# Kernel tuning notes

Measured on AMD Instinct MI355X. Metric: run time of the kernel, lower is better.

The kernel has to match this reference:

```python
import jax, jax.numpy as jnp
import numpy as np

N = 100000
NFEAT = 512
NHID = 256
NCLASS = 40
E = 1600000
K = 10          # nlayers propagation hops
ALPHA = 0.1


def setup_inputs() -> dict:
    key = jax.random.key(0)
    ks = jax.random.split(key, 8)
    x = jax.random.normal(ks[0], (N, NFEAT), dtype=jnp.float32)
    edge_src = jax.random.randint(ks[1], (E,), 0, N, dtype=jnp.int32)
    edge_dst = jax.random.randint(ks[2], (E,), 0, N, dtype=jnp.int32)
    # roughly row-stochastic-scale edge values (avg degree ~16)
    edge_val = jax.random.uniform(ks[3], (E,), dtype=jnp.float32) * (1.0 / 16.0)
    stdv1 = 1.0 / np.sqrt(NFEAT)
    W1 = jax.random.uniform(ks[4], (NFEAT, NHID), minval=-stdv1, maxval=stdv1, dtype=jnp.float32)
    b1 = jax.random.uniform(ks[5], (NHID,), minval=-stdv1, maxval=stdv1, dtype=jnp.float32)
    stdv2 = 1.0 / np.sqrt(NHID)
    W2 = jax.random.uniform(ks[6], (NHID, NCLASS), minval=-stdv2, maxval=stdv2, dtype=jnp.float32)
    b2 = jax.random.uniform(ks[7], (NCLASS,), minval=-stdv2, maxval=stdv2, dtype=jnp.float32)
    return {"x": x, "edge_src": edge_src, "edge_dst": edge_dst, "edge_val": edge_val,
            "W1": W1, "b1": b1, "W2": W2, "b2": b2}


def _spmm(edge_src, edge_dst, edge_val, z):
    # sparse adj @ z via gather + segment-sum scatter: out[dst] += val * z[src]
    msgs = edge_val[:, None] * z[edge_src]          # [E, C]
    return jax.ops.segment_sum(msgs, edge_dst, num_segments=N)


def reference(x, edge_src, edge_dst, edge_val, W1, b1, W2, b2):
    # MLP transform (dropout is identity in eval mode)
    h = jax.nn.relu(x @ W1 + b1)                    # [N, NHID]
    h = h @ W2 + b2                                 # [N, NCLASS]
    # APPNP propagation: z <- (1-alpha) * A z + alpha * h
    def step(z, _):
        z = _spmm(edge_src, edge_dst, edge_val, z) * (1.0 - ALPHA) + ALPHA * h
        return z, None
    z, _ = jax.lax.scan(step, h, None, length=K)
    return jax.nn.log_softmax(z, axis=1)
```

## Files before the change

kernel.cpp:

```cpp
#include <hip/hip_runtime.h>
#include <hip/hip_bf16.h>
#include <math.h>

#define NN     100000
#define NFEATD 512
#define NHIDD  256
#define NCLS   40
#define NE     1600000
#define KHOP   10

typedef __attribute__((ext_vector_type(8))) short short8;
typedef __attribute__((ext_vector_type(4))) float floatx4;

static __device__ __forceinline__ float bf2f(unsigned int u) {
  unsigned int x = u << 16;
  float f;
  __builtin_memcpy(&f, &x, 4);
  return f;
}
static __device__ __forceinline__ unsigned short f2bf(float f) {
  unsigned int x;
  __builtin_memcpy(&x, &f, 4);
  x = (x + 0x7fffu + ((x >> 16) & 1u)) >> 16;
  return (unsigned short)x;
}
static __device__ __forceinline__ void bf8_to_f(const uint4 u, float* f) {
  unsigned int a0 = u.x, a1 = u.y, a2 = u.z, a3 = u.w;
  unsigned int t;
  t = a0 << 16;          __builtin_memcpy(&f[0], &t, 4);
  t = a0 & 0xffff0000u;  __builtin_memcpy(&f[1], &t, 4);
  t = a1 << 16;          __builtin_memcpy(&f[2], &t, 4);
  t = a1 & 0xffff0000u;  __builtin_memcpy(&f[3], &t, 4);
  t = a2 << 16;          __builtin_memcpy(&f[4], &t, 4);
  t = a2 & 0xffff0000u;  __builtin_memcpy(&f[5], &t, 4);
  t = a3 << 16;          __builtin_memcpy(&f[6], &t, 4);
  t = a3 & 0xffff0000u;  __builtin_memcpy(&f[7], &t, 4);
}

__global__ __launch_bounds__(256) void wt_kernel(const float* __restrict__ W1,
                                                 unsigned short* __restrict__ Wt) {
  int i = blockIdx.x * 256 + threadIdx.x;
  int k = i >> 8;
  int n = i & 255;
  Wt[n * 512 + k] = f2bf(W1[i]);
}

__global__ __launch_bounds__(256) void gemm1_mfma_kernel(
    const float* __restrict__ x, const unsigned short* __restrict__ Wt,
    const float* __restrict__ b1, unsigned short* __restrict__ h1) {
  __shared__ unsigned short As[128 * 40];
  __shared__ unsigned short Bs[128 * 40];
  const int tid = threadIdx.x;
  const int lane = tid & 63;
  const int wave = tid >> 6;
  const int wr = wave >> 1, wc = wave & 1;
  const int m = lane & 15, quad = lane >> 4;
  const int c0 = blockIdx.x * 128;
  const int r0 = blockIdx.y * 128;

  const int arow = tid >> 3;
  const int akq = tid & 7;
  const int brow = tid >> 2;
  const int bkq = tid & 3;

  floatx4 acc[4][4];
#pragma unroll
  for (int i = 0; i < 4; ++i)
#pragma unroll
    for (int j = 0; j < 4; ++j) acc[i][j] = (floatx4){0.f, 0.f, 0.f, 0.f};

  float4 aR[4];
  uint4 bR[2];
#pragma unroll
  for (int rep = 0; rep < 4; ++rep) {
    int grow = r0 + arow + rep * 32;
    aR[rep] = make_float4(0.f, 0.f, 0.f, 0.f);
    if (grow < NN) aR[rep] = *(const float4*)(x + grow * NFEATD + akq * 4);
  }
#pragma unroll
  for (int rep = 0; rep < 2; ++rep)
    bR[rep] = *(const uint4*)(Wt + (c0 + brow + rep * 64) * NFEATD + bkq * 8);

  for (int kt = 0; kt < NFEATD; kt += 32) {
#pragma unroll
    for (int rep = 0; rep < 4; ++rep) {
      ushort4 o;
      o.x = f2bf(aR[rep].x);
      o.y = f2bf(aR[rep].y);
      o.z = f2bf(aR[rep].z);
      o.w = f2bf(aR[rep].w);
      *(ushort4*)&As[(arow + rep * 32) * 40 + akq * 4] = o;
    }
#pragma unroll
    for (int rep = 0; rep < 2; ++rep)
      *(uint4*)&Bs[(brow + rep * 64) * 40 + bkq * 8] = bR[rep];
    __syncthreads();

    int ktn = kt + 32;
    if (ktn < NFEATD) {
#pragma unroll
      for (int rep = 0; rep < 4; ++rep) {
        int grow = r0 + arow + rep * 32;
        float4 v = make_float4(0.f, 0.f, 0.f, 0.f);
        if (grow < NN) v = *(const float4*)(x + grow * NFEATD + ktn + akq * 4);
        aR[rep] = v;
      }
#pragma unroll
      for (int rep = 0; rep < 2; ++rep)
        bR[rep] = *(const uint4*)(Wt + (c0 + brow + rep * 64) * NFEATD + ktn + bkq * 8);
    }

    short8 af[4], bfr[4];
#pragma unroll
    for (int i = 0; i < 4; ++i)
      af[i] = *(const short8*)&As[(wr * 64 + i * 16 + m) * 40 + quad * 8];
#pragma unroll
    for (int j = 0; j < 4; ++j)
      bfr[j] = *(const short8*)&Bs[(wc * 64 + j * 16 + m) * 40 + quad * 8];
#pragma unroll
    for (int i = 0; i < 4; ++i)
#pragma unroll
      for (int j = 0; j < 4; ++j)
        acc[i][j] = __builtin_amdgcn_mfma_f32_16x16x32_bf16(af[i], bfr[j], acc[i][j], 0, 0, 0);
    __syncthreads();
  }

  float bias[4];
#pragma unroll
  for (int j = 0; j < 4; ++j) bias[j] = b1[c0 + wc * 64 + j * 16 + m];
#pragma unroll
  for (int i = 0; i < 4; ++i) {
#pragma unroll
    for (int r = 0; r < 4; ++r) {
      int row = r0 + wr * 64 + i * 16 + quad * 4 + r;
      if (row < NN) {
#pragma unroll
        for (int j = 0; j < 4; ++j) {
          float v = acc[i][j][r] + bias[j];
          h1[row * NHIDD + c0 + wc * 64 + j * 16 + m] = f2bf(fmaxf(v, 0.f));
        }
      }
    }
  }
}

__global__ __launch_bounds__(256) void gemm2_kernel(
    const unsigned short* __restrict__ h1, const float* __restrict__ W2,
    const float* __restrict__ b2, unsigned short* __restrict__ hb) {
  __shared__ float w2s[NHIDD * NCLS];
  __shared__ float b2s[NCLS];
  __shared__ unsigned short h1s[64 * 264];
  const int tid = threadIdx.x;
  const int r0 = blockIdx.x * 64;
  for (int i = tid; i < NHIDD * NCLS; i += 256) w2s[i] = W2[i];
  if (tid < NCLS) b2s[tid] = b2[tid];
#pragma unroll
  for (int q = 0; q < 8; ++q) {
    int l = tid + q * 256;
    int lr = l >> 5;
    int lc = (l & 31) << 3;
    int row = r0 + lr;
    uint4 v = make_uint4(0, 0, 0, 0);
    if (row < NN) v = *(const uint4*)(h1 + row * NHIDD + lc);
    *(uint4*)&h1s[lr * 264 + lc] = v;
  }
  __syncthreads();
  const int lr = tid >> 2;
  const int cq = (tid & 3) * 10;
  float acc[10];
#pragma unroll
  for (int j = 0; j < 10; ++j) acc[j] = 0.f;
#pragma unroll 4
  for (int k = 0; k < NHIDD; k += 2) {
    unsigned int hp = *(const unsigned int*)&h1s[lr * 264 + k];
    float a0 = bf2f(hp & 0xffffu);
    float a1 = bf2f(hp >> 16);
    const float* w0 = &w2s[k * NCLS + cq];
    const float* w1 = &w2s[(k + 1) * NCLS + cq];
#pragma unroll
    for (int j = 0; j < 10; ++j)
      acc[j] = fmaf(a1, w1[j], fmaf(a0, w0[j], acc[j]));
  }
  int row = r0 + lr;
  if (row < NN) {
#pragma unroll
    for (int jj = 0; jj < 5; ++jj) {
      unsigned int u = (unsigned int)f2bf(acc[2 * jj] + b2s[cq + 2 * jj]) |
                       ((unsigned int)f2bf(acc[2 * jj + 1] + b2s[cq + 2 * jj + 1]) << 16);
      *(unsigned int*)&hb[row * NCLS + cq + 2 * jj] = u;
    }
  }
}

__global__ __launch_bounds__(256) void zero_kernel(int* __restrict__ p, int n) {
  int i = blockIdx.x * 256 + threadIdx.x;
  if (i < n) p[i] = 0;
}
__global__ __launch_bounds__(256) void count_kernel(const int* __restrict__ edst,
                                                    int* __restrict__ counts) {
  int e = blockIdx.x * 256 + threadIdx.x;
  if (e < NE) atomicAdd(&counts[edst[e]], 1);
}
__global__ __launch_bounds__(256) void hist_kernel(const int* __restrict__ counts,
                                                   int* __restrict__ binoff) {
  __shared__ int lhist[64];
  int tid = threadIdx.x;
  if (tid < 64) lhist[tid] = 0;
  __syncthreads();
  int r = blockIdx.x * 256 + tid;
  if (r < NN) {
    int d = counts[r];
    if (d > 63) d = 63;
    atomicAdd(&lhist[d], 1);
  }
  __syncthreads();
  if (tid < 64) {
    int c = lhist[tid];
    if (c) atomicAdd(&binoff[tid], c);
  }
}
__global__ __launch_bounds__(64) void binscan_kernel(int* __restrict__ binoff) {
  __shared__ int s[64];
  int t = threadIdx.x;
  s[t] = binoff[t];
  __syncthreads();
  if (t == 0) {
    int run = 0;
    for (int i = 0; i < 64; ++i) {
      int c = s[i];
      s[i] = run;
      run += c;
    }
  }
  __syncthreads();
  binoff[t] = s[t];
}
__global__ __launch_bounds__(256) void scatter_rows_kernel(
    const int* __restrict__ counts, int* __restrict__ binoff,
    int* __restrict__ perm, int* __restrict__ spos) {
  __shared__ int lhist[64];
  __shared__ int lbase[64];
  int tid = threadIdx.x;
  if (tid < 64) lhist[tid] = 0;
  __syncthreads();
  int r = blockIdx.x * 256 + tid;
  int d = 0, lrank = 0;
  bool valid = (r < NN);
  if (valid) {
    d = counts[r];
    if (d > 63) d = 63;
    lrank = atomicAdd(&lhist[d], 1);
  }
  __syncthreads();
  if (tid < 64) {
    int c = lhist[tid];
    lbase[tid] = c ? atomicAdd(&binoff[tid], c) : 0;
  }
  __syncthreads();
  if (valid) {
    int pos = lbase[d] + lrank;
    perm[pos] = r;
    spos[r] = pos;
  }
}
__global__ __launch_bounds__(256) void scan_blocks_kernel(
    const int* __restrict__ counts, const int* __restrict__ perm,
    int* __restrict__ srs, int* __restrict__ bsum) {
  __shared__ int s[256];
  int gid = blockIdx.x * 256 + threadIdx.x;
  int v = (gid < NN) ? counts[perm[gid]] : 0;
  s[threadIdx.x] = v;
  __syncthreads();
  for (int off = 1; off < 256; off <<= 1) {
    int t = (threadIdx.x >= off) ? s[threadIdx.x - off] : 0;
    __syncthreads();
    s[threadIdx.x] += t;
    __syncthreads();
  }
  if (gid < NN) srs[gid + 1] = s[threadIdx.x];
  if (threadIdx.x == 255) bsum[blockIdx.x] = s[255];
}
#define NB 391
__global__ __launch_bounds__(512) void scan_sums_kernel(int* __restrict__ bsum) {
  __shared__ int s[512];
  int tid = threadIdx.x;
  int v = (tid < NB) ? bsum[tid] : 0;
  s[tid] = v;
  __syncthreads();
  for (int off = 1; off < 512; off <<= 1) {
    int t = (tid >= off) ? s[tid - off] : 0;
    __syncthreads();
    s[tid] += t;
    __syncthreads();
  }
  if (tid < NB) bsum[tid] = (tid == 0) ? 0 : s[tid - 1];
}
__global__ __launch_bounds__(256) void add_off_kernel(int* __restrict__ srs,
                                                      const int* __restrict__ bsum) {
  int gid = blockIdx.x * 256 + threadIdx.x;
  if (gid < NN) srs[gid + 1] += bsum[blockIdx.x];
  if (gid == 0) srs[0] = 0;
}
__global__ __launch_bounds__(256) void scatter_kernel(
    const int* __restrict__ esrc, const int* __restrict__ edst,
    const float* __restrict__ eval, const int* __restrict__ srs,
    const int* __restrict__ spos, int* __restrict__ cursor,
    int2* __restrict__ csr_pair) {
  int e = blockIdx.x * 256 + threadIdx.x;
  if (e < NE) {
    int p = spos[edst[e]];
    int idx = srs[p] + atomicAdd(&cursor[p], 1);
    csr_pair[idx] = make_int2(esrc[e], __float_as_int(eval[e]));
  }
}

__global__ __launch_bounds__(256) void prop_kernel(
    const int* __restrict__ srs, const int* __restrict__ perm,
    const int2* __restrict__ csr_pair, const unsigned short* __restrict__ zi,
    const unsigned short* __restrict__ hb, unsigned short* __restrict__ zo) {
  int t = blockIdx.x * 256 + threadIdx.x;
  if (t >= NN * 5) return;
  unsigned int p = (unsigned int)t / 5u;
  int cg8 = (t - (int)p * 5) * 8;
  int e0 = srs[p], e1 = srs[p + 1];
  int r = perm[p];
  float acc[8];
#pragma unroll
  for (int j = 0; j < 8; ++j) acc[j] = 0.f;

  int e = e0;
  for (; e + 8 <= e1; e += 8) {
    int2 pr[8];
#pragma unroll
    for (int q = 0; q < 8; ++q) pr[q] = csr_pair[e + q];
    uint4 g[8];
#pragma unroll
    for (int q = 0; q < 8; ++q)
      g[q] = *(const uint4*)(zi + pr[q].x * NCLS + cg8);
#pragma unroll
    for (int q = 0; q < 8; ++q) {
      float zf[8];
      bf8_to_f(g[q], zf);
      float v = __int_as_float(pr[q].y);
#pragma unroll
      for (int j = 0; j < 8; ++j) acc[j] = fmaf(v, zf[j], acc[j]);
    }
  }
  for (; e < e1; ++e) {
    int2 pr = csr_pair[e];
    uint4 g = *(const uint4*)(zi + pr.x * NCLS + cg8);
    float zf[8];
    bf8_to_f(g, zf);
    float v = __int_as_float(pr.y);
#pragma unroll
    for (int j = 0; j < 8; ++j) acc[j] = fmaf(v, zf[j], acc[j]);
  }

  uint4 hu = *(const uint4*)(hb + r * NCLS + cg8);
  float hf[8];
  bf8_to_f(hu, hf);
  uint4 o;
  unsigned int w[4];
#pragma unroll
  for (int i = 0; i < 4; ++i) {
    unsigned int lo = f2bf(0.9f * acc[2 * i] + 0.1f * hf[2 * i]);
    unsigned int hi = f2bf(0.9f * acc[2 * i + 1] + 0.1f * hf[2 * i + 1]);
    w[i] = lo | (hi << 16);
  }
  o.x = w[0];
  o.y = w[1];
  o.z = w[2];
  o.w = w[3];
  *(uint4*)(zo + r * NCLS + cg8) = o;
}

__global__ __launch_bounds__(256) void lsm_kernel(const unsigned short* __restrict__ zf,
                                                  float* __restrict__ out) {
  int r = blockIdx.x * 256 + threadIdx.x;
  if (r >= NN) return;
  float v[NCLS];
#pragma unroll
  for (int q = 0; q < 5; ++q) {
    uint4 u = *(const uint4*)(zf + r * NCLS + q * 8);
    bf8_to_f(u, v + q * 8);
  }
  float m = v[0];
#pragma unroll
  for (int i = 1; i < NCLS; ++i) m = fmaxf(m, v[i]);
  float ssum = 0.f;
#pragma unroll
  for (int i = 0; i < NCLS; ++i) ssum += expf(v[i] - m);
  float lse = m + logf(ssum);
#pragma unroll
  for (int q = 0; q < 10; ++q) {
    float4 o;
    o.x = v[q * 4 + 0] - lse;
    o.y = v[q * 4 + 1] - lse;
    o.z = v[q * 4 + 2] - lse;
    o.w = v[q * 4 + 3] - lse;
    *(float4*)(out + r * NCLS + q * 4) = o;
  }
}

extern "C" void kernel_launch(void* const* d_in, const int* in_sizes, int n_in,
                              void* d_out, int out_size, void* d_ws, size_t ws_size,
                              hipStream_t stream) {
  const float* x = (const float*)d_in[0];
  const int* esrc = (const int*)d_in[1];
  const int* edst = (const int*)d_in[2];
  const float* eval = (const float*)d_in[3];
  const float* W1 = (const float*)d_in[4];
  const float* b1 = (const float*)d_in[5];
  const float* W2 = (const float*)d_in[6];
  const float* b2 = (const float*)d_in[7];
  float* out = (float*)d_out;
  char* ws = (char*)d_ws;

  unsigned short* hb = (unsigned short*)(ws + 0);
  unsigned short* zB0 = (unsigned short*)(ws + 8000000);
  unsigned short* zB1 = (unsigned short*)(ws + 16000000);
  unsigned short* Wt = (unsigned short*)(ws + 24000000);
  unsigned short* h1 = (unsigned short*)(ws + 24400000);
  int* counts = (int*)(ws + 75600000);
  int* cursor = (int*)(ws + 76000000);
  int* srs = (int*)(ws + 76400000);
  int* bsum = (int*)(ws + 76800064);
  int* binoff = (int*)(ws + 76802112);
  int* perm = (int*)(ws + 76802624);
  int* spos = (int*)(ws + 77202624);
  int2* csr_pair = (int2*)(ws + 77602624);

  zero_kernel<<<(2 * NN + 255) / 256, 256, 0, stream>>>(counts, 2 * NN);
  zero_kernel<<<1, 256, 0, stream>>>(binoff, 64);

  wt_kernel<<<(NFEATD * NHIDD) / 256, 256, 0, stream>>>(W1, Wt);
  gemm1_mfma_kernel<<<dim3(2, (NN + 127) / 128), 256, 0, stream>>>(x, Wt, b1, h1);
  gemm2_kernel<<<(NN + 63) / 64, 256, 0, stream>>>(h1, W2, b2, hb);

  count_kernel<<<(NE + 255) / 256, 256, 0, stream>>>(edst, counts);
  hist_kernel<<<(NN + 255) / 256, 256, 0, stream>>>(counts, binoff);
  binscan_kernel<<<1, 64, 0, stream>>>(binoff);
  scatter_rows_kernel<<<(NN + 255) / 256, 256, 0, stream>>>(counts, binoff, perm, spos);
  scan_blocks_kernel<<<NB, 256, 0, stream>>>(counts, perm, srs, bsum);
  scan_sums_kernel<<<1, 512, 0, stream>>>(bsum);
  add_off_kernel<<<NB, 256, 0, stream>>>(srs, bsum);
  scatter_kernel<<<(NE + 255) / 256, 256, 0, stream>>>(esrc, edst, eval, srs, spos,
                                                       cursor, csr_pair);

  const unsigned short* zin = hb;
  unsigned short* zout = zB0;
  for (int i = 0; i < KHOP; ++i) {
    prop_kernel<<<(NN * 5 + 255) / 256, 256, 0, stream>>>(srs, perm, csr_pair,
                                                          zin, hb, zout);
    if (i == 0) {
      zin = zB0;
      zout = zB1;
    } else {
      unsigned short* t = (unsigned short*)zin;
      zin = zout;
      zout = t;
    }
  }

  lsm_kernel<<<(NN + 255) / 256, 256, 0, stream>>>(zB1, out);
}
```

Measured before the change: 1.038 ms.

## Stream GEMM1 operands directly from global memory into MFMA fragments

Measured after the change: 1.072 ms. +3.3%, slower.

```diff
diff --git a/kernel.cpp b/kernel.cpp
--- a/kernel.cpp
+++ b/kernel.cpp
@@ -45,102 +45,107 @@
   Wt[n * 512 + k] = f2bf(W1[i]);
 }
 
-__global__ __launch_bounds__(256) void gemm1_mfma_kernel(
+__global__ __launch_bounds__(256) void gemm1_stream_kernel(
     const float* __restrict__ x, const unsigned short* __restrict__ Wt,
     const float* __restrict__ b1, unsigned short* __restrict__ h1) {
-  __shared__ unsigned short As[128 * 40];
-  __shared__ unsigned short Bs[128 * 40];
+  __shared__ __align__(16) unsigned short hs[128 * 128];
   const int tid = threadIdx.x;
   const int lane = tid & 63;
-  const int wave = tid >> 6;
-  const int wr = wave >> 1, wc = wave & 1;
-  const int m = lane & 15, quad = lane >> 4;
-  const int c0 = blockIdx.x * 128;
-  const int r0 = blockIdx.y * 128;
-
-  const int arow = tid >> 3;
-  const int akq = tid & 7;
-  const int brow = tid >> 2;
-  const int bkq = tid & 3;
-
-  floatx4 acc[4][4];
-#pragma unroll
-  for (int i = 0; i < 4; ++i)
-#pragma unroll
-    for (int j = 0; j < 4; ++j) acc[i][j] = (floatx4){0.f, 0.f, 0.f, 0.f};
-
-  float4 aR[4];
-  uint4 bR[2];
-#pragma unroll
-  for (int rep = 0; rep < 4; ++rep) {
-    int grow = r0 + arow + rep * 32;
-    aR[rep] = make_float4(0.f, 0.f, 0.f, 0.f);
-    if (grow < NN) aR[rep] = *(const float4*)(x + grow * NFEATD + akq * 4);
-  }
-#pragma unroll
-  for (int rep = 0; rep < 2; ++rep)
-    bR[rep] = *(const uint4*)(Wt + (c0 + brow + rep * 64) * NFEATD + bkq * 8);
-
-  for (int kt = 0; kt < NFEATD; kt += 32) {
-#pragma unroll
-    for (int rep = 0; rep < 4; ++rep) {
-      ushort4 o;
-      o.x = f2bf(aR[rep].x);
-      o.y = f2bf(aR[rep].y);
-      o.z = f2bf(aR[rep].z);
-      o.w = f2bf(aR[rep].w);
-      *(ushort4*)&As[(arow + rep * 32) * 40 + akq * 4] = o;
-    }
-#pragma unroll
-    for (int rep = 0; rep < 2; ++rep)
-      *(uint4*)&Bs[(brow + rep * 64) * 40 + bkq * 8] = bR[rep];
-    __syncthreads();
-
-    int ktn = kt + 32;
-    if (ktn < NFEATD) {
-#pragma unroll
-      for (int rep = 0; rep < 4; ++rep) {
-        int grow = r0 + arow + rep * 32;
-        float4 v = make_float4(0.f, 0.f, 0.f, 0.f);
-        if (grow < NN) v = *(const float4*)(x + grow * NFEATD + ktn + akq * 4);
-        aR[rep] = v;
+  const int w = tid >> 6;
+  const int m = lane & 15;
+  const int q = lane >> 4;
+
+  int b = blockIdx.x;
+  int g = b >> 4, slot = b & 15;
+  int xcol = slot >> 3;
+  int y = g * 8 + (slot & 7);
+  if (y >= 782) return;
+  const int r0 = y * 128 + w * 32;
+  const int c0 = xcol * 128;
+
+  const float* arow[2];
+#pragma unroll
+  for (int i = 0; i < 2; ++i) {
+    int gr = r0 + i * 16 + m;
+    arow[i] = x + (size_t)(gr < NN ? gr : 0) * NFEATD + q * 8;
+  }
+  const unsigned short* brow = Wt + (c0 + m) * NFEATD + q * 8;
+
+  floatx4 acc[2][8];
+#pragma unroll
+  for (int i = 0; i < 2; ++i)
+#pragma unroll
+    for (int j = 0; j < 8; ++j) acc[i][j] = (floatx4){0.f, 0.f, 0.f, 0.f};
+
+  float4 apf[2][2][2];
+#pragma unroll
+  for (int par = 0; par < 2; ++par)
+#pragma unroll
+    for (int i = 0; i < 2; ++i) {
+      apf[par][i][0] = *(const float4*)(arow[i] + par * 32);
+      apf[par][i][1] = *(const float4*)(arow[i] + par * 32 + 4);
+    }
+
+#pragma unroll
+  for (int s = 0; s < 16; ++s) {
+    const int par = s & 1;
+    short8 bfr[8];
+#pragma unroll
+    for (int j = 0; j < 8; ++j)
+      bfr[j] = *(const short8*)(brow + j * 16 * NFEATD + s * 32);
+    short8 af[2];
+#pragma unroll
+    for (int i = 0; i < 2; ++i) {
+      float4 lo = apf[par][i][0], hi = apf[par][i][1];
+      short8 t;
+      t[0] = (short)f2bf(lo.x);
+      t[1] = (short)f2bf(lo.y);
+      t[2] = (short)f2bf(lo.z);
+      t[3] = (short)f2bf(lo.w);
+      t[4] = (short)f2bf(hi.x);
+      t[5] = (short)f2bf(hi.y);
+      t[6] = (short)f2bf(hi.z);
+      t[7] = (short)f2bf(hi.w);
+      af[i] = t;
+    }
+    if (s + 2 < 16) {
+#pragma unroll
+      for (int i = 0; i < 2; ++i) {
+        apf[par][i][0] = *(const float4*)(arow[i] + (s + 2) * 32);
+        apf[par][i][1] = *(const float4*)(arow[i] + (s + 2) * 32 + 4);
       }
-#pragma unroll
-      for (int rep = 0; rep < 2; ++rep)
-        bR[rep] = *(const uint4*)(Wt + (c0 + brow + rep * 64) * NFEATD + ktn + bkq * 8);
-    }
-
-    short8 af[4], bfr[4];
-#pragma unroll
-    for (int i = 0; i < 4; ++i)
-      af[i] = *(const short8*)&As[(wr * 64 + i * 16 + m) * 40 + quad * 8];
-#pragma unroll
-    for (int j = 0; j < 4; ++j)
-      bfr[j] = *(const short8*)&Bs[(wc * 64 + j * 16 + m) * 40 + quad * 8];
-#pragma unroll
-    for (int i = 0; i < 4; ++i)
-#pragma unroll
-      for (int j = 0; j < 4; ++j)
-        acc[i][j] = __builtin_amdgcn_mfma_f32_16x16x32_bf16(af[i], bfr[j], acc[i][j], 0, 0, 0);
-    __syncthreads();
-  }
-
-  float bias[4];
-#pragma unroll
-  for (int j = 0; j < 4; ++j) bias[j] = b1[c0 + wc * 64 + j * 16 + m];
-#pragma unroll
-  for (int i = 0; i < 4; ++i) {
+    }
+#pragma unroll
+    for (int i = 0; i < 2; ++i)
+#pragma unroll
+      for (int j = 0; j < 8; ++j)
+        acc[i][j] =
+            __builtin_amdgcn_mfma_f32_16x16x32_bf16(af[i], bfr[j], acc[i][j], 0, 0, 0);
+  }
+
+  float bias[8];
+#pragma unroll
+  for (int j = 0; j < 8; ++j) bias[j] = b1[c0 + j * 16 + m];
+#pragma unroll
+  for (int i = 0; i < 2; ++i)
 #pragma unroll
     for (int r = 0; r < 4; ++r) {
-      int row = r0 + wr * 64 + i * 16 + quad * 4 + r;
-      if (row < NN) {
-#pragma unroll
-        for (int j = 0; j < 4; ++j) {
-          float v = acc[i][j][r] + bias[j];
-          h1[row * NHIDD + c0 + wc * 64 + j * 16 + m] = f2bf(fmaxf(v, 0.f));
-        }
+      int rl = w * 32 + i * 16 + q * 4 + r;
+#pragma unroll
+      for (int j = 0; j < 8; ++j) {
+        float v = acc[i][j][r] + bias[j];
+        hs[rl * 128 + j * 16 + m] = f2bf(fmaxf(v, 0.f));
       }
     }
+  __syncthreads();
+#pragma unroll
+  for (int rep = 0; rep < 8; ++rep) {
+    int idx = rep * 256 + tid;
+    int row = idx >> 4;
+    int grow = y * 128 + row;
+    uint4 v = *(const uint4*)&hs[idx * 8];
+    if (grow < NN)
+      *(uint4*)(h1 + grow * NHIDD + c0 + (idx & 15) * 8) = v;
   }
 }
 
@@ -360,17 +365,17 @@
   float hf[8];
   bf8_to_f(hu, hf);
   uint4 o;
-  unsigned int w[4];
+  unsigned int wv[4];
 #pragma unroll
   for (int i = 0; i < 4; ++i) {
     unsigned int lo = f2bf(0.9f * acc[2 * i] + 0.1f * hf[2 * i]);
     unsigned int hi = f2bf(0.9f * acc[2 * i + 1] + 0.1f * hf[2 * i + 1]);
-    w[i] = lo | (hi << 16);
-  }
-  o.x = w[0];
-  o.y = w[1];
-  o.z = w[2];
-  o.w = w[3];
+    wv[i] = lo | (hi << 16);
+  }
+  o.x = wv[0];
+  o.y = wv[1];
+  o.z = wv[2];
+  o.w = wv[3];
   *(uint4*)(zo + r * NCLS + cg8) = o;
 }
 
@@ -434,7 +439,7 @@
   zero_kernel<<<1, 256, 0, stream>>>(binoff, 64);
 
   wt_kernel<<<(NFEATD * NHIDD) / 256, 256, 0, stream>>>(W1, Wt);
-  gemm1_mfma_kernel<<<dim3(2, (NN + 127) / 128), 256, 0, stream>>>(x, Wt, b1, h1);
+  gemm1_stream_kernel<<<1568, 256, 0, stream>>>(x, Wt, b1, h1);
   gemm2_kernel<<<(NN + 63) / 64, 256, 0, stream>>>(h1, W2, b2, hb);
 
   count_kernel<<<(NE + 255) / 256, 256, 0, stream>>>(edst, counts);
```

## Double-buffer LDS in gemm1 and stage output through shared memory

Applied to the files above, without the earlier changes.

New measurement: 1.049 ms. About the same (+1.1%).

```diff
diff --git a/kernel.cpp b/kernel.cpp
--- a/kernel.cpp
+++ b/kernel.cpp
@@ -48,8 +48,12 @@
 __global__ __launch_bounds__(256) void gemm1_mfma_kernel(
     const float* __restrict__ x, const unsigned short* __restrict__ Wt,
     const float* __restrict__ b1, unsigned short* __restrict__ h1) {
-  __shared__ unsigned short As[128 * 40];
-  __shared__ unsigned short Bs[128 * 40];
+  __shared__ __align__(16) unsigned short smem_u[20480];
+  unsigned short* As0 = smem_u;
+  unsigned short* Bs0 = smem_u + 5120;
+  unsigned short* As1 = smem_u + 10240;
+  unsigned short* Bs1 = smem_u + 15360;
+  unsigned short* hs = smem_u;
   const int tid = threadIdx.x;
   const int lane = tid & 63;
   const int wave = tid >> 6;
@@ -69,79 +73,110 @@
 #pragma unroll
     for (int j = 0; j < 4; ++j) acc[i][j] = (floatx4){0.f, 0.f, 0.f, 0.f};
 
-  float4 aR[4];
-  uint4 bR[2];
+  const float* asrc[4];
 #pragma unroll
   for (int rep = 0; rep < 4; ++rep) {
     int grow = r0 + arow + rep * 32;
-    aR[rep] = make_float4(0.f, 0.f, 0.f, 0.f);
-    if (grow < NN) aR[rep] = *(const float4*)(x + grow * NFEATD + akq * 4);
-  }
+    asrc[rep] = x + (size_t)(grow < NN ? grow : 0) * NFEATD + akq * 4;
+  }
+  const unsigned short* bsrc[2];
 #pragma unroll
   for (int rep = 0; rep < 2; ++rep)
-    bR[rep] = *(const uint4*)(Wt + (c0 + brow + rep * 64) * NFEATD + bkq * 8);
-
-  for (int kt = 0; kt < NFEATD; kt += 32) {
-#pragma unroll
-    for (int rep = 0; rep < 4; ++rep) {
-      ushort4 o;
-      o.x = f2bf(aR[rep].x);
-      o.y = f2bf(aR[rep].y);
-      o.z = f2bf(aR[rep].z);
-      o.w = f2bf(aR[rep].w);
-      *(ushort4*)&As[(arow + rep * 32) * 40 + akq * 4] = o;
-    }
-#pragma unroll
-    for (int rep = 0; rep < 2; ++rep)
-      *(uint4*)&Bs[(brow + rep * 64) * 40 + bkq * 8] = bR[rep];
-    __syncthreads();
-
-    int ktn = kt + 32;
-    if (ktn < NFEATD) {
-#pragma unroll
-      for (int rep = 0; rep < 4; ++rep) {
-        int grow = r0 + arow + rep * 32;
-        float4 v = make_float4(0.f, 0.f, 0.f, 0.f);
-        if (grow < NN) v = *(const float4*)(x + grow * NFEATD + ktn + akq * 4);
-        aR[rep] = v;
-      }
-#pragma unroll
-      for (int rep = 0; rep < 2; ++rep)
-        bR[rep] = *(const uint4*)(Wt + (c0 + brow + rep * 64) * NFEATD + ktn + bkq * 8);
-    }
-
-    short8 af[4], bfr[4];
-#pragma unroll
-    for (int i = 0; i < 4; ++i)
-      af[i] = *(const short8*)&As[(wr * 64 + i * 16 + m) * 40 + quad * 8];
-#pragma unroll
-    for (int j = 0; j < 4; ++j)
-      bfr[j] = *(const short8*)&Bs[(wc * 64 + j * 16 + m) * 40 + quad * 8];
-#pragma unroll
-    for (int i = 0; i < 4; ++i)
+    bsrc[rep] = Wt + (size_t)(c0 + brow + rep * 64) * NFEATD + bkq * 8;
+
+#define LOAD_A(dst, koff)                                        \
+  {                                                              \
+    _Pragma("unroll") for (int rep = 0; rep < 4; ++rep)          \
+        dst[rep] = *(const float4*)(asrc[rep] + (koff));         \
+  }
+#define LOAD_B(dst, koff)                                        \
+  {                                                              \
+    _Pragma("unroll") for (int rep = 0; rep < 2; ++rep)          \
+        dst[rep] = *(const uint4*)(bsrc[rep] + (koff));          \
+  }
+#define STAGE(Ad, Bd, aregs, bregs)                              \
+  {                                                              \
+    _Pragma("unroll") for (int rep = 0; rep < 4; ++rep) {        \
+      ushort4 o;                                                 \
+      o.x = f2bf(aregs[rep].x);                                  \
+      o.y = f2bf(aregs[rep].y);                                  \
+      o.z = f2bf(aregs[rep].z);                                  \
+      o.w = f2bf(aregs[rep].w);                                  \
+      *(ushort4*)&Ad[(arow + rep * 32) * 40 + akq * 4] = o;      \
+    }                                                            \
+    _Pragma("unroll") for (int rep = 0; rep < 2; ++rep)          \
+        *(uint4*)&Bd[(brow + rep * 64) * 40 + bkq * 8] = bregs[rep]; \
+  }
+#define COMPUTE(Asb, Bsb)                                        \
+  {                                                              \
+    short8 af[4], bfr[4];                                        \
+    _Pragma("unroll") for (int i = 0; i < 4; ++i)                \
+        af[i] = *(const short8*)&Asb[(wr * 64 + i * 16 + m) * 40 + quad * 8]; \
+    _Pragma("unroll") for (int j = 0; j < 4; ++j)                \
+        bfr[j] = *(const short8*)&Bsb[(wc * 64 + j * 16 + m) * 40 + quad * 8]; \
+    _Pragma("unroll") for (int i = 0; i < 4; ++i)                \
+        _Pragma("unroll") for (int j = 0; j < 4; ++j)            \
+            acc[i][j] = __builtin_amdgcn_mfma_f32_16x16x32_bf16( \
+                af[i], bfr[j], acc[i][j], 0, 0, 0);              \
+  }
+#define BAR()                                                    \
+  {                                                              \
+    asm volatile("s_waitcnt lgkmcnt(0)" ::: "memory");           \
+    __builtin_amdgcn_s_barrier();                                \
+  }
+
+  float4 aA[4], aB[4];
+  uint4 bA[2], bB[2];
+  LOAD_A(aA, 0); LOAD_B(bA, 0);
+  LOAD_A(aB, 32); LOAD_B(bB, 32);
+  STAGE(As0, Bs0, aA, bA);
+  BAR();
+  LOAD_A(aA, 64); LOAD_B(bA, 64);
+
+#pragma unroll 1
+  for (int t = 0; t < 8; ++t) {
+    const int kt = t * 64;
+    STAGE(As1, Bs1, aB, bB);
+    if (t < 7) { LOAD_A(aB, kt + 96); LOAD_B(bB, kt + 96); }
+    COMPUTE(As0, Bs0);
+    BAR();
+    if (t < 7) {
+      STAGE(As0, Bs0, aA, bA);
+      if (t < 6) { LOAD_A(aA, kt + 128); LOAD_B(bA, kt + 128); }
+    }
+    COMPUTE(As1, Bs1);
+    BAR();
+  }
+
+  float bias[4];
+#pragma unroll
+  for (int j = 0; j < 4; ++j) bias[j] = b1[c0 + wc * 64 + j * 16 + m];
+#pragma unroll
+  for (int i = 0; i < 4; ++i)
+#pragma unroll
+    for (int r = 0; r < 4; ++r) {
+      int rl = wr * 64 + i * 16 + quad * 4 + r;
 #pragma unroll
       for (int j = 0; j < 4; ++j)
-        acc[i][j] = __builtin_amdgcn_mfma_f32_16x16x32_bf16(af[i], bfr[j], acc[i][j], 0, 0, 0);
-    __syncthreads();
-  }
-
-  float bias[4];
-#pragma unroll
-  for (int j = 0; j < 4; ++j) bias[j] = b1[c0 + wc * 64 + j * 16 + m];
-#pragma unroll
-  for (int i = 0; i < 4; ++i) {
-#pragma unroll
-    for (int r = 0; r < 4; ++r) {
-      int row = r0 + wr * 64 + i * 16 + quad * 4 + r;
-      if (row < NN) {
-#pragma unroll
-        for (int j = 0; j < 4; ++j) {
-          float v = acc[i][j][r] + bias[j];
-          h1[row * NHIDD + c0 + wc * 64 + j * 16 + m] = f2bf(fmaxf(v, 0.f));
-        }
-      }
-    }
-  }
+        hs[rl * 128 + wc * 64 + j * 16 + m] =
+            f2bf(fmaxf(acc[i][j][r] + bias[j], 0.f));
+    }
+  BAR();
+#pragma unroll
+  for (int rep = 0; rep < 8; ++rep) {
+    int idx = rep * 256 + tid;
+    int row = idx >> 4;
+    int grow = r0 + row;
+    if (grow < NN) {
+      uint4 v = *(const uint4*)&hs[idx * 8];
+      *(uint4*)(h1 + (size_t)grow * NHIDD + c0 + (idx & 15) * 8) = v;
+    }
+  }
+#undef LOAD_A
+#undef LOAD_B
+#undef STAGE
+#undef COMPUTE
+#undef BAR
 }
 
 __global__ __launch_bounds__(256) void gemm2_kernel(
@@ -152,7 +187,9 @@
   __shared__ unsigned short h1s[64 * 264];
   const int tid = threadIdx.x;
   const int r0 = blockIdx.x * 64;
-  for (int i = tid; i < NHIDD * NCLS; i += 256) w2s[i] = W2[i];
+#pragma unroll
+  for (int i = 0; i < 10; ++i)
+    ((float4*)w2s)[tid + i * 256] = ((const float4*)W2)[tid + i * 256];
   if (tid < NCLS) b2s[tid] = b2[tid];
 #pragma unroll
   for (int q = 0; q < 8; ++q) {
@@ -161,7 +198,7 @@
     int lc = (l & 31) << 3;
     int row = r0 + lr;
     uint4 v = make_uint4(0, 0, 0, 0);
-    if (row < NN) v = *(const uint4*)(h1 + row * NHIDD + lc);
+    if (row < NN) v = *(const uint4*)(h1 + (size_t)row * NHIDD + lc);
     *(uint4*)&h1s[lr * 264 + lc] = v;
   }
   __syncthreads();
@@ -178,8 +215,12 @@
     const float* w0 = &w2s[k * NCLS + cq];
     const float* w1 = &w2s[(k + 1) * NCLS + cq];
 #pragma unroll
-    for (int j = 0; j < 10; ++j)
-      acc[j] = fmaf(a1, w1[j], fmaf(a0, w0[j], acc[j]));
+    for (int j2 = 0; j2 < 5; ++j2) {
+      float2 wa = *(const float2*)(w0 + 2 * j2);
+      float2 wb = *(const float2*)(w1 + 2 * j2);
+      acc[2 * j2] = fmaf(a1, wb.x, fmaf(a0, wa.x, acc[2 * j2]));
+      acc[2 * j2 + 1] = fmaf(a1, wb.y, fmaf(a0, wa.y, acc[2 * j2 + 1]));
+    }
   }
   int row = r0 + lr;
   if (row < NN) {
@@ -187,7 +228,7 @@
     for (int jj = 0; jj < 5; ++jj) {
       unsigned int u = (unsigned int)f2bf(acc[2 * jj] + b2s[cq + 2 * jj]) |
                        ((unsigned int)f2bf(acc[2 * jj + 1] + b2s[cq + 2 * jj + 1]) << 16);
-      *(unsigned int*)&hb[row * NCLS + cq + 2 * jj] = u;
+      *(unsigned int*)&hb[(size_t)row * NCLS + cq + 2 * jj] = u;
     }
   }
 }
@@ -360,17 +401,17 @@
   float hf[8];
   bf8_to_f(hu, hf);
   uint4 o;
-  unsigned int w[4];
+  unsigned int wv[4];
 #pragma unroll
   for (int i = 0; i < 4; ++i) {
     unsigned int lo = f2bf(0.9f * acc[2 * i] + 0.1f * hf[2 * i]);
     unsigned int hi = f2bf(0.9f * acc[2 * i + 1] + 0.1f * hf[2 * i + 1]);
-    w[i] = lo | (hi << 16);
-  }
-  o.x = w[0];
-  o.y = w[1];
-  o.z = w[2];
-  o.w = w[3];
+    wv[i] = lo | (hi << 16);
+  }
+  o.x = wv[0];
+  o.y = wv[1];
+  o.z = wv[2];
+  o.w = wv[3];
   *(uint4*)(zo + r * NCLS + cg8) = o;
 }
 
```
